# Performance work log

Hardware: AMD Instinct MI355X
Metric: run time of the kernel (lower is better)

Reference implementation:

```python
import jax, jax.numpy as jnp
import numpy as np

# dims: batch, time, in-feat, nodes, hidden, out-feat, filter taps, readout widths
BATCH, T, F, N, H, G = 8, 64, 8, 4096, 32, 32
K1, K2 = 3, 3
R1, R2 = 64, 8


def lsigf(h, S, x):
    """K-tap graph filter (LSIGF, E=1): h (Fout,K,Fin), S (N,N), x (B,Fin,N) -> (B,Fout,N)."""
    K = h.shape[1]
    xs = [x]
    for _ in range(K - 1):  # K is small and static
        xs.append(jnp.einsum('nm,bfm->bfn', S, xs[-1]))
    xk = jnp.stack(xs, axis=1)  # B,K,Fin,N
    return jnp.einsum('gkf,bkfn->bgn', h, xk)


def setup_inputs() -> dict:
    key = jax.random.key(0)
    ks = jax.random.split(key, 20)
    def p(k, shape, scale):
        return jax.random.normal(k, shape, dtype=jnp.float32) * scale
    x = jax.random.normal(ks[0], (BATCH, T, F, N), dtype=jnp.float32)
    z0 = jax.random.normal(ks[1], (BATCH, H, N), dtype=jnp.float32)  # random initial hidden state
    S = jax.random.normal(ks[2], (N, N), dtype=jnp.float32) / jnp.sqrt(jnp.float32(N))  # GSO, O(1) spectral norm
    sA = 1.0 / np.sqrt(K1 * F); sB = 1.0 / np.sqrt(K1 * H); sO = 1.0 / np.sqrt(K2 * H)
    return dict(
        x=x, z0=z0, S=S,
        # main hidden-state filters
        A=p(ks[3], (H, K1, F), sA), Bw=p(ks[4], (H, K1, H), sB), bz=p(ks[5], (H, 1), 0.1),
        # input (update) time-gate filters
        Ca=p(ks[6], (H, K1, F), sA), Cb=p(ks[7], (H, K1, H), sB), bc=p(ks[8], (H, 1), 0.1),
        # forget time-gate filters
        Da=p(ks[9], (H, K1, F), sA), Db=p(ks[10], (H, K1, H), sB), bd=p(ks[11], (H, 1), 0.1),
        # output graph filter
        Wout=p(ks[12], (G, K2, H), sO), bout=p(ks[13], (G, 1), 0.1),
        # local per-node readout MLP G -> R1 -> R2
        W1=p(ks[14], (R1, G), 1.0 / np.sqrt(G)), b1=p(ks[15], (R1,), 0.1),
        W2=p(ks[16], (R2, R1), 1.0 / np.sqrt(R1)), b2=p(ks[17], (R2,), 0.1),
    )


def reference(x, z0, S, A, Bw, bz, Ca, Cb, bc, Da, Db, bd, Wout, bout, W1, b1, W2, b2):
    Bsz = x.shape[0]
    xt_seq = jnp.moveaxis(x, 1, 0)  # T,B,F,N

    def step(z, xt):
        # scalar-per-(batch,time) gates: sigmoid of gate graph filters, pooled over nodes+features
        u = jax.nn.sigmoid(lsigf(Ca, S, xt) + lsigf(Cb, S, z) + bc).mean(axis=(1, 2))[:, None, None]
        f = jax.nn.sigmoid(lsigf(Da, S, xt) + lsigf(Db, S, z) + bd).mean(axis=(1, 2))[:, None, None]
        znew = jnp.tanh(u * lsigf(A, S, xt) + f * lsigf(Bw, S, z) + bz)
        return znew, znew

    _, zs = jax.lax.scan(step, z0, xt_seq)  # T,B,H,N
    z = jnp.moveaxis(zs, 0, 1).reshape(Bsz * T, H, N)
    yOut = jnp.tanh(lsigf(Wout, S, z) + bout).reshape(Bsz, T, G, N)  # nonlinearityOutput = tanh
    y = jnp.moveaxis(yOut, 2, 3)  # B,T,N,G  (local per-node readout)
    y = jax.nn.relu(y @ W1.T + b1) @ W2.T + b2  # B,T,N,R2
    return jnp.moveaxis(y, 3, 2)  # B,T,R2,N
```

## Files before the change

kernel.cpp:

```cpp
#include <hip/hip_runtime.h>
#include <hip/hip_bf16.h>
#include <cstdio>

typedef __attribute__((ext_vector_type(4))) float f32x4;
typedef __attribute__((ext_vector_type(8))) short bf16x8;

__device__ __forceinline__ short f2b(float f) {
  unsigned u = __builtin_bit_cast(unsigned, f);
  unsigned r = (u + 0x7FFFu + ((u >> 16) & 1u)) >> 16;
  return (short)r;
}
__device__ __forceinline__ float b2f(short s) {
  union { unsigned u; float f; } c;
  c.u = ((unsigned)(unsigned short)s) << 16;
  return c.f;
}
__device__ __forceinline__ float sigm(float x) { return 1.f / (1.f + __expf(-x)); }
__device__ __forceinline__ float tanh_f(float x) {
  float e = __expf(2.f * x);
  return 1.f - 2.f / (e + 1.f);
}

#define GLOAD16(gp, lp) \
  __builtin_amdgcn_global_load_lds((__attribute__((address_space(1))) const void*)(gp), \
                                   (__attribute__((address_space(3))) void*)(lp), 16, 0, 0)


__global__ void conv_k(const float* __restrict__ in, short* __restrict__ out, int n8) {
  int i = blockIdx.x * 256 + threadIdx.x;
  if (i >= n8) return;
  size_t base = (size_t)i * 8;
  f32x4 a = *(const f32x4*)(in + base), b = *(const f32x4*)(in + base + 4);
  bf16x8 v;
#pragma unroll
  for (int j = 0; j < 4; ++j) { v[j] = f2b(a[j]); v[4 + j] = f2b(b[j]); }
  *(bf16x8*)(out + base) = v;
}

__global__ void transpose_k(const float* __restrict__ in, short* __restrict__ out) {
  __shared__ float tile[32][33];
  int bx = blockIdx.x * 32, by = blockIdx.y * 32;
  int tx = threadIdx.x, ty = threadIdx.y;
  for (int i = ty; i < 32; i += 8)
    tile[i][tx] = in[(size_t)(by + i) * 4096 + bx + tx];
  __syncthreads();
  for (int i = ty; i < 32; i += 8)
    out[(size_t)(bx + i) * 4096 + by + tx] = f2b(tile[tx][i]);
}

template <int AF32>
__global__ __launch_bounds__(256) void gemm_big(const void* __restrict__ Av,
                                                const short* __restrict__ Bt,
                                                short* __restrict__ C,
                                                int K, int ldc) {
  __shared__ __align__(16) short Ab[2][128 * 64];
  __shared__ __align__(16) short Bb[2][128 * 64];
  const int tid = threadIdx.x, lane = tid & 63, w = tid >> 6;
  const int wm = w >> 1, wn = w & 1;
  const int r16 = lane & 15, g4 = lane >> 4;
  const size_t m0 = (size_t)blockIdx.y * 128, n0 = (size_t)blockIdx.x * 128;
  const int lrow8 = lane >> 3;
  const int lslot = (lane & 7) ^ lrow8;
  const int swz = r16 & 7;
  const int arow = tid >> 1, acol0 = (tid & 1) * 32, aslotb = (tid & 1) * 4;

  f32x4 acc[4][4];
#pragma unroll
  for (int mi = 0; mi < 4; ++mi)
#pragma unroll
    for (int ni = 0; ni < 4; ++ni) acc[mi][ni] = (f32x4)0.f;

  auto stageB = [&](int bs, int kt) {
#pragma unroll
    for (int i = 0; i < 4; ++i) {
      int chunk = w * 4 + i, row = chunk * 8 + lrow8;
      GLOAD16(&Bt[(size_t)(n0 + row) * K + kt + lslot * 8], &Bb[bs][chunk * 512]);
    }
  };
  auto stageA16 = [&](int bs, int kt) {
    const short* A = (const short*)Av;
#pragma unroll
    for (int i = 0; i < 4; ++i) {
      int chunk = w * 4 + i, row = chunk * 8 + lrow8;
      GLOAD16(&A[(size_t)(m0 + row) * K + kt + lslot * 8], &Ab[bs][chunk * 512]);
    }
  };
  auto writeA32 = [&](int bs, const f32x4* st) {
#pragma unroll
    for (int s = 0; s < 4; ++s) {
      bf16x8 v;
#pragma unroll
      for (int e = 0; e < 4; ++e) { v[e] = f2b(st[s * 2][e]); v[4 + e] = f2b(st[s * 2 + 1][e]); }
      int ps = (aslotb + s) ^ (arow & 7);
      *(bf16x8*)&Ab[bs][arow * 64 + ps * 8] = v;
    }
  };

  const float* A32 = (const float*)Av;
  if (AF32) {
    f32x4 st[8];
#pragma unroll
    for (int j = 0; j < 8; ++j)
      st[j] = *(const f32x4*)&A32[(m0 + arow) * (size_t)K + acol0 + j * 4];
    stageB(0, 0);
    writeA32(0, st);
  } else {
    stageA16(0, 0);
    stageB(0, 0);
  }
  __syncthreads();

  int cur = 0;
  for (int kt = 0; kt < K; kt += 64) {
    const bool nxt = (kt + 64 < K);
    f32x4 st[8];
    if (nxt) {
      if (AF32) {
#pragma unroll
        for (int j = 0; j < 8; ++j)
          st[j] = *(const f32x4*)&A32[(m0 + arow) * (size_t)K + kt + 64 + acol0 + j * 4];
      } else {
        stageA16(cur ^ 1, kt + 64);
      }
      stageB(cur ^ 1, kt + 64);
    }
#pragma unroll
    for (int ks = 0; ks < 2; ++ks) {
      const int so = ((ks * 4 + g4) ^ swz) * 8;
      bf16x8 af[4], bf[4];
#pragma unroll
      for (int i = 0; i < 4; ++i) {
        af[i] = *(const bf16x8*)&Ab[cur][(wm * 64 + i * 16 + r16) * 64 + so];
        bf[i] = *(const bf16x8*)&Bb[cur][(wn * 64 + i * 16 + r16) * 64 + so];
      }
#pragma unroll
      for (int mi = 0; mi < 4; ++mi)
#pragma unroll
        for (int ni = 0; ni < 4; ++ni)
          acc[mi][ni] = __builtin_amdgcn_mfma_f32_16x16x32_bf16(af[mi], bf[ni], acc[mi][ni], 0, 0, 0);
    }
    if (nxt && AF32) writeA32(cur ^ 1, st);
    __syncthreads();
    cur ^= 1;
  }
#pragma unroll
  for (int mi = 0; mi < 4; ++mi) {
#pragma unroll
    for (int ni = 0; ni < 4; ++ni) {
      size_t row0 = m0 + wm * 64 + mi * 16 + g4 * 4;
      size_t col  = n0 + wn * 64 + ni * 16 + r16;
#pragma unroll
      for (int r = 0; r < 4; ++r)
        C[(row0 + r) * (size_t)ldc + col] = f2b(acc[mi][ni][r]);
    }
  }
}

__global__ __launch_bounds__(512, 1) void step_fused(
    const short* __restrict__ zbuf, const short* __restrict__ Scat,
    const float* __restrict__ x, const short* __restrict__ xsh,
    const float* __restrict__ Ca, const float* __restrict__ Cb, const float* __restrict__ bc,
    const float* __restrict__ Da, const float* __restrict__ Db, const float* __restrict__ bd,
    const float* __restrict__ Af, const float* __restrict__ Bw,
    const float* __restrict__ Wout, const float* __restrict__ bout,
    const float* __restrict__ W1, const float* __restrict__ b1,
    const float* __restrict__ W2, const float* __restrict__ b2,
    float* __restrict__ zab, float* __restrict__ gacc,
    float* __restrict__ out, int t) {
  __shared__ __align__(16) char smem[118624];
  short* AbB = (short*)smem;
  short* BbB = (short*)(smem + 32768);
  short* Cs  = (short*)smem;
  short* zs  = (short*)(smem + 18432);
  float* Fu  = (float*)(smem + 49152);
  float* Fd  = (float*)(smem + 64512);
  float* Fb  = (float*)(smem + 79872);
  float* Fa  = (float*)(smem + 92160);
  float* Wc  = (float*)(smem + 95232);
  float* W1L = (float*)(smem + 107520);
  float* W2L = (float*)(smem + 115712);
  float* bcs   = (float*)(smem + 117760);
  float* bds   = (float*)(smem + 117888);
  float* boutL = (float*)(smem + 118144);
  float* b1L   = (float*)(smem + 118272);
  float* b2L   = (float*)(smem + 118528);
  float* red   = (float*)(smem + 118560);

  const int tid = threadIdx.x, lane = tid & 63, w = tid >> 6;
  const int wm = w >> 1, wn = w & 1;
  const int r16 = lane & 15, g4 = lane >> 4;
  const int lrow8 = lane >> 3;
  const int lslot = (lane & 7) ^ lrow8;
  const int swz = r16 & 7;
  const int mhalf = blockIdx.x >> 7, ntile = blockIdx.x & 127;
  const int m0 = mhalf << 7, n0 = ntile << 5;

  for (int i = tid; i < 3840; i += 512) {
    int j = i >> 5, h = i & 31; float fu, fd;
    if (j < 96) { int k = j >> 5, hh = j & 31;
      fu = Cb[(h * 3 + k) * 32 + hh]; fd = Db[(h * 3 + k) * 32 + hh]; }
    else { int jj = j - 96, k = jj >> 3, f = jj & 7;
      fu = Ca[(h * 3 + k) * 8 + f];  fd = Da[(h * 3 + k) * 8 + f]; }
    Fu[i] = fu; Fd[i] = fd;
  }
  for (int i = tid; i < 3072; i += 512) { int j = i >> 5, h = i & 31, k = j >> 5, hh = j & 31;
    Fb[i] = Bw[(h * 3 + k) * 32 + hh]; }
  for (int i = tid; i < 768;  i += 512) { int j = i >> 5, h = i & 31, k = j >> 3, f = j & 7;
    Fa[i] = Af[(h * 3 + k) * 8 + f]; }
  for (int i = tid; i < 3072; i += 512) { int j = i >> 5, g = i & 31, k = j >> 5, hh = j & 31;
    Wc[i] = Wout[(g * 3 + k) * 32 + hh]; }
  for (int i = tid; i < 2048; i += 512) { int r1 = i >> 5, g = i & 31; W1L[i] = W1[r1 * 32 + g]; }
  if (tid < 512) { int r1 = tid >> 3, r = tid & 7; W2L[tid] = W2[r * 64 + r1]; }
  if (tid < 32) { bcs[tid] = bc[tid]; bds[tid] = bd[tid]; boutL[tid] = bout[tid]; }
  if (tid < 64) b1L[tid] = b1[tid];
  if (tid < 8)  b2L[tid] = b2[tid];
  __syncthreads();

  const short* z = zbuf + (size_t)(t & 1) * 1048576;

  f32x4 acc[2][2];
  acc[0][0] = acc[0][1] = acc[1][0] = acc[1][1] = (f32x4)0.f;
  auto stage = [&](int bs, int kt) {
#pragma unroll
    for (int i = 0; i < 2; ++i) {
      int chunk = w * 2 + i, row = chunk * 8 + lrow8;
      GLOAD16(&z[(size_t)(m0 + row) * 4096 + kt + lslot * 8], &AbB[bs * 8192 + chunk * 512]);
    }
    { int row = w * 8 + lrow8;
      int grow = (row < 32) ? (n0 + row) : (4064 + n0 + row);
      GLOAD16(&Scat[(size_t)grow * 4096 + kt + lslot * 8], &BbB[bs * 4096 + w * 512]); }
  };
  stage(0, 0);
  __syncthreads();
  int cur = 0;
  for (int kt = 0; kt < 4096; kt += 64) {
    if (kt + 64 < 4096) stage(cur ^ 1, kt + 64);
#pragma unroll
    for (int ks = 0; ks < 2; ++ks) {
      const int so = ((ks * 4 + g4) ^ swz) * 8;
      bf16x8 af[2], bb[2];
#pragma unroll
      for (int i = 0; i < 2; ++i) {
        af[i] = *(const bf16x8*)&AbB[cur * 8192 + (wm * 32 + i * 16 + r16) * 64 + so];
        bb[i] = *(const bf16x8*)&BbB[cur * 4096 + (wn * 32 + i * 16 + r16) * 64 + so];
      }
#pragma unroll
      for (int mi = 0; mi < 2; ++mi)
#pragma unroll
        for (int ni = 0; ni < 2; ++ni)
          acc[mi][ni] = __builtin_amdgcn_mfma_f32_16x16x32_bf16(af[mi], bb[ni], acc[mi][ni], 0, 0, 0);
    }
    __syncthreads();
    cur ^= 1;
  }
#pragma unroll
  for (int mi = 0; mi < 2; ++mi)
#pragma unroll
    for (int ni = 0; ni < 2; ++ni) {
      int row0 = wm * 32 + mi * 16 + g4 * 4, col = wn * 32 + ni * 16 + r16;
#pragma unroll
      for (int rr = 0; rr < 4; ++rr)
        Cs[(row0 + rr) * 72 + col] = f2b(acc[mi][ni][rr]);
    }
  { int row = tid >> 2, c0 = (tid & 3) * 8;
    *(bf16x8*)&zs[row * 40 + c0] = *(const bf16x8*)&z[(size_t)(m0 + row) * 4096 + n0 + c0]; }
  __syncthreads();

  if (t >= 1 && tid < 128) {
    int b_loc = tid >> 5, nn = tid & 31;
    int b_glob = (mhalf << 2) + b_loc;
    f32x4 oa[8];
#pragma unroll
    for (int q = 0; q < 8; ++q) oa[q] = (f32x4)0.f;
    for (int j = 0; j < 96; ++j) {
      int k = j >> 5, hh = j & 31;
      float v = (k == 0) ? b2f(zs[(b_loc * 32 + hh) * 40 + nn])
                         : b2f(Cs[(b_loc * 32 + hh) * 72 + (k - 1) * 32 + nn]);
#pragma unroll
      for (int q = 0; q < 8; ++q) oa[q] += (*(const f32x4*)&Wc[j * 32 + q * 4]) * v;
    }
    f32x4 y[8];
#pragma unroll
    for (int q = 0; q < 8; ++q)
#pragma unroll
      for (int c = 0; c < 4; ++c) y[q][c] = tanh_f(oa[q][c] + boutL[q * 4 + c]);
    f32x4 o0 = { b2L[0], b2L[1], b2L[2], b2L[3] };
    f32x4 o1 = { b2L[4], b2L[5], b2L[6], b2L[7] };
    for (int r1 = 0; r1 < 64; ++r1) {
      f32x4 p = y[0] * (*(const f32x4*)&W1L[r1 * 32]);
#pragma unroll
      for (int q = 1; q < 8; ++q) p += y[q] * (*(const f32x4*)&W1L[r1 * 32 + q * 4]);
      float hv = b1L[r1] + p[0] + p[1] + p[2] + p[3];
      hv = fmaxf(hv, 0.f);
      o0 += (*(const f32x4*)&W2L[r1 * 8]) * hv;
      o1 += (*(const f32x4*)&W2L[r1 * 8 + 4]) * hv;
    }
    size_t obase = ((size_t)(b_glob * 64 + (t - 1)) * 8) * 4096 + n0 + nn;
#pragma unroll
    for (int rr = 0; rr < 4; ++rr) {
      out[obase + (size_t)rr * 4096]       = o0[rr];
      out[obase + (size_t)(4 + rr) * 4096] = o1[rr];
    }
  }

  if (t < 64) {
    int nn = tid & 31; int q = tid >> 5; int b_loc = q >> 2; int h0 = (q & 3) * 8;
    int b_glob = (mhalf << 2) + b_loc;
    int n = n0 + nn;
    f32x4 zaA = (f32x4)0.f, zaB = (f32x4)0.f, zbA = (f32x4)0.f, zbB = (f32x4)0.f;
    f32x4 guA = *(const f32x4*)&bcs[h0], guB = *(const f32x4*)&bcs[h0 + 4];
    f32x4 gdA = *(const f32x4*)&bds[h0], gdB = *(const f32x4*)&bds[h0 + 4];
    for (int j = 0; j < 96; ++j) {
      int k = j >> 5, hh = j & 31;
      float v = (k == 0) ? b2f(zs[(b_loc * 32 + hh) * 40 + nn])
                         : b2f(Cs[(b_loc * 32 + hh) * 72 + (k - 1) * 32 + nn]);
      guA += (*(const f32x4*)&Fu[j * 32 + h0]) * v;  guB += (*(const f32x4*)&Fu[j * 32 + h0 + 4]) * v;
      gdA += (*(const f32x4*)&Fd[j * 32 + h0]) * v;  gdB += (*(const f32x4*)&Fd[j * 32 + h0 + 4]) * v;
      zbA += (*(const f32x4*)&Fb[j * 32 + h0]) * v;  zbB += (*(const f32x4*)&Fb[j * 32 + h0 + 4]) * v;
    }
    size_t xr = ((size_t)b_glob * 64 + t) * 8;
    for (int j = 0; j < 24; ++j) {
      int k = j >> 3, f = j & 7;
      float v = (k == 0) ? x[(xr + f) * 4096 + n]
                         : b2f(xsh[(xr + f) * 8192 + (size_t)(k - 1) * 4096 + n]);
      guA += (*(const f32x4*)&Fu[(96 + j) * 32 + h0]) * v;  guB += (*(const f32x4*)&Fu[(96 + j) * 32 + h0 + 4]) * v;
      gdA += (*(const f32x4*)&Fd[(96 + j) * 32 + h0]) * v;  gdB += (*(const f32x4*)&Fd[(96 + j) * 32 + h0 + 4]) * v;
      zaA += (*(const f32x4*)&Fa[j * 32 + h0]) * v;         zaB += (*(const f32x4*)&Fa[j * 32 + h0 + 4]) * v;
    }
    float su = 0.f, sd = 0.f;
    size_t zr = (size_t)(b_glob * 32 + h0) * 4096 + n;
#pragma unroll
    for (int i = 0; i < 4; ++i) {
      su += sigm(guA[i]) + sigm(guB[i]);
      sd += sigm(gdA[i]) + sigm(gdB[i]);
      zab[zr + (size_t)i * 4096]                 = zaA[i];
      zab[zr + (size_t)(4 + i) * 4096]           = zaB[i];
      zab[1048576 + zr + (size_t)i * 4096]       = zbA[i];
      zab[1048576 + zr + (size_t)(4 + i) * 4096] = zbB[i];
    }
#pragma unroll
    for (int off = 32; off; off >>= 1) { su += __shfl_down(su, off); sd += __shfl_down(sd, off); }
    if (lane == 0) { red[w * 2] = su; red[w * 2 + 1] = sd; }
    __syncthreads();
    if (tid < 4) {
      int par = t & 1, bg = (mhalf << 2) + tid;
      atomicAdd(&gacc[par * 16 + bg],     red[4 * tid] + red[4 * tid + 2]);
      atomicAdd(&gacc[par * 16 + 8 + bg], red[4 * tid + 1] + red[4 * tid + 3]);
    }
  }
}

__global__ __launch_bounds__(256) void update_kernel(
    const float* __restrict__ zab, float* __restrict__ gacc,
    const float* __restrict__ bz, short* __restrict__ zout, int t) {
  const int par = t & 1;
  if (blockIdx.x == 0 && threadIdx.x < 16) gacc[(par ^ 1) * 16 + threadIdx.x] = 0.f;
  size_t idx = (size_t)blockIdx.x * 256 + threadIdx.x;
  size_t base = idx * 8;
  int row = (int)(base >> 12);
  int b = row >> 5, h = row & 31;
  float u  = gacc[par * 16 + b]     * (1.f / 131072.f);
  float fg = gacc[par * 16 + 8 + b] * (1.f / 131072.f);
  float bzv = bz[h];
  f32x4 za0 = *(const f32x4*)(zab + base),           za1 = *(const f32x4*)(zab + base + 4);
  f32x4 zb0 = *(const f32x4*)(zab + 1048576 + base), zb1 = *(const f32x4*)(zab + 1048576 + base + 4);
  bf16x8 ov;
#pragma unroll
  for (int i = 0; i < 4; ++i) {
    ov[i]     = f2b(tanh_f(u * za0[i] + fg * zb0[i] + bzv));
    ov[4 + i] = f2b(tanh_f(u * za1[i] + fg * zb1[i] + bzv));
  }
  *(bf16x8*)(zout + base) = ov;
}

extern "C" void kernel_launch(void* const* d_in, const int* in_sizes, int n_in,
                              void* d_out, int out_size, void* d_ws, size_t ws_size,
                              hipStream_t stream) {
  const float* x    = (const float*)d_in[0];
  const float* z0   = (const float*)d_in[1];
  const float* S    = (const float*)d_in[2];
  const float* Af   = (const float*)d_in[3];
  const float* Bw   = (const float*)d_in[4];
  const float* bz   = (const float*)d_in[5];
  const float* Ca   = (const float*)d_in[6];
  const float* Cb   = (const float*)d_in[7];
  const float* bc   = (const float*)d_in[8];
  const float* Da   = (const float*)d_in[9];
  const float* Db   = (const float*)d_in[10];
  const float* bd   = (const float*)d_in[11];
  const float* Wout = (const float*)d_in[12];
  const float* bo   = (const float*)d_in[13];
  const float* W1   = (const float*)d_in[14];
  const float* b1   = (const float*)d_in[15];
  const float* W2   = (const float*)d_in[16];
  const float* b2   = (const float*)d_in[17];
  float* out = (float*)d_out;

  char* w = (char*)d_ws;
  short* Scat = (short*)w; w += (size_t)8192 * 4096 * 2;
  short* xsh  = (short*)w; w += (size_t)4096 * 8192 * 2;
  short* zbuf = (short*)w; w += (size_t)2 * 1048576 * 2;
  float* zab  = (float*)w; w += (size_t)2 * 1048576 * 4;
  float* gacc = (float*)w; w += 256;
  size_t need = (size_t)(w - (char*)d_ws);
  if (ws_size < need) {
    fprintf(stderr, "kernel_launch: WS TOO SMALL need=%zu have=%zu -- NOT LAUNCHING\n",
            need, ws_size);
    return;
  }

  short* STt = xsh;

  conv_k<<<512, 256, 0, stream>>>(z0, zbuf, 131072);
  conv_k<<<8192, 256, 0, stream>>>(S, Scat, 2097152);
  transpose_k<<<dim3(128, 128), dim3(32, 8), 0, stream>>>(S, STt);
  gemm_big<0><<<dim3(32, 32), 256, 0, stream>>>(Scat, STt, Scat + (size_t)4096 * 4096, 4096, 4096);
  gemm_big<1><<<dim3(64, 32), 256, 0, stream>>>(x, Scat, xsh, 4096, 8192);
  hipMemsetAsync(gacc, 0, 256, stream);

  for (int t = 0; t <= 64; ++t) {
    short* znxt = zbuf + (size_t)((t + 1) & 1) * 1048576;
    step_fused<<<256, 512, 0, stream>>>(zbuf, Scat, x, xsh,
                                        Ca, Cb, bc, Da, Db, bd, Af, Bw,
                                        Wout, bo, W1, b1, W2, b2,
                                        zab, gacc, out, t);
    if (t < 64)
      update_kernel<<<512, 256, 0, stream>>>(zab, gacc, bz, znxt, t);
  }
}
```

Before: 6.905 ms.

## Triple-buffer step kernel GEMM loads and simplify precompute GEMM staging

```diff
diff --git a/kernel.cpp b/kernel.cpp
--- a/kernel.cpp
+++ b/kernel.cpp
@@ -49,20 +49,17 @@
 }
 
 template <int AF32>
-__global__ __launch_bounds__(256) void gemm_big(const void* __restrict__ Av,
+__global__ __launch_bounds__(256) void gemm_pre(const void* __restrict__ Av,
                                                 const short* __restrict__ Bt,
                                                 short* __restrict__ C,
                                                 int K, int ldc) {
-  __shared__ __align__(16) short Ab[2][128 * 64];
-  __shared__ __align__(16) short Bb[2][128 * 64];
-  const int tid = threadIdx.x, lane = tid & 63, w = tid >> 6;
-  const int wm = w >> 1, wn = w & 1;
+  __shared__ __align__(16) short As[128][72];
+  __shared__ __align__(16) short Bs[128][72];
+  const int tid = threadIdx.x;
+  const int lane = tid & 63, wave = tid >> 6;
+  const int wm = wave >> 1, wn = wave & 1;
+  const size_t m0 = (size_t)blockIdx.y * 128, n0 = (size_t)blockIdx.x * 128;
   const int r16 = lane & 15, g4 = lane >> 4;
-  const size_t m0 = (size_t)blockIdx.y * 128, n0 = (size_t)blockIdx.x * 128;
-  const int lrow8 = lane >> 3;
-  const int lslot = (lane & 7) ^ lrow8;
-  const int swz = r16 & 7;
-  const int arow = tid >> 1, acol0 = (tid & 1) * 32, aslotb = (tid & 1) * 4;
 
   f32x4 acc[4][4];
 #pragma unroll
@@ -70,78 +67,42 @@
 #pragma unroll
     for (int ni = 0; ni < 4; ++ni) acc[mi][ni] = (f32x4)0.f;
 
-  auto stageB = [&](int bs, int kt) {
-#pragma unroll
-    for (int i = 0; i < 4; ++i) {
-      int chunk = w * 4 + i, row = chunk * 8 + lrow8;
-      GLOAD16(&Bt[(size_t)(n0 + row) * K + kt + lslot * 8], &Bb[bs][chunk * 512]);
-    }
-  };
-  auto stageA16 = [&](int bs, int kt) {
-    const short* A = (const short*)Av;
-#pragma unroll
-    for (int i = 0; i < 4; ++i) {
-      int chunk = w * 4 + i, row = chunk * 8 + lrow8;
-      GLOAD16(&A[(size_t)(m0 + row) * K + kt + lslot * 8], &Ab[bs][chunk * 512]);
-    }
-  };
-  auto writeA32 = [&](int bs, const f32x4* st) {
-#pragma unroll
-    for (int s = 0; s < 4; ++s) {
-      bf16x8 v;
-#pragma unroll
-      for (int e = 0; e < 4; ++e) { v[e] = f2b(st[s * 2][e]); v[4 + e] = f2b(st[s * 2 + 1][e]); }
-      int ps = (aslotb + s) ^ (arow & 7);
-      *(bf16x8*)&Ab[bs][arow * 64 + ps * 8] = v;
-    }
-  };
-
-  const float* A32 = (const float*)Av;
-  if (AF32) {
-    f32x4 st[8];
-#pragma unroll
-    for (int j = 0; j < 8; ++j)
-      st[j] = *(const f32x4*)&A32[(m0 + arow) * (size_t)K + acol0 + j * 4];
-    stageB(0, 0);
-    writeA32(0, st);
-  } else {
-    stageA16(0, 0);
-    stageB(0, 0);
-  }
-  __syncthreads();
-
-  int cur = 0;
   for (int kt = 0; kt < K; kt += 64) {
-    const bool nxt = (kt + 64 < K);
-    f32x4 st[8];
-    if (nxt) {
+#pragma unroll
+    for (int r = 0; r < 4; ++r) {
+      int idx = r * 256 + tid;
+      int row = idx >> 3;
+      int kin = (idx & 7) * 8;
       if (AF32) {
-#pragma unroll
-        for (int j = 0; j < 8; ++j)
-          st[j] = *(const f32x4*)&A32[(m0 + arow) * (size_t)K + kt + 64 + acol0 + j * 4];
+        const float* A = (const float*)Av;
+        const float* p = &A[(m0 + row) * (size_t)K + kt + kin];
+        f32x4 a = *(const f32x4*)p, b = *(const f32x4*)(p + 4);
+        bf16x8 v;
+#pragma unroll
+        for (int j = 0; j < 4; ++j) { v[j] = f2b(a[j]); v[4 + j] = f2b(b[j]); }
+        *(bf16x8*)&As[row][kin] = v;
       } else {
-        stageA16(cur ^ 1, kt + 64);
+        const short* A = (const short*)Av;
+        *(bf16x8*)&As[row][kin] = *(const bf16x8*)&A[(m0 + row) * (size_t)K + kt + kin];
       }
-      stageB(cur ^ 1, kt + 64);
-    }
+      *(bf16x8*)&Bs[row][kin] = *(const bf16x8*)&Bt[(n0 + row) * (size_t)K + kt + kin];
+    }
+    __syncthreads();
 #pragma unroll
     for (int ks = 0; ks < 2; ++ks) {
-      const int so = ((ks * 4 + g4) ^ swz) * 8;
-      bf16x8 af[4], bf[4];
+      bf16x8 af[4], bfr[4];
 #pragma unroll
       for (int i = 0; i < 4; ++i) {
-        af[i] = *(const bf16x8*)&Ab[cur][(wm * 64 + i * 16 + r16) * 64 + so];
-        bf[i] = *(const bf16x8*)&Bb[cur][(wn * 64 + i * 16 + r16) * 64 + so];
+        af[i]  = *(const bf16x8*)&As[wm * 64 + i * 16 + r16][ks * 32 + g4 * 8];
+        bfr[i] = *(const bf16x8*)&Bs[wn * 64 + i * 16 + r16][ks * 32 + g4 * 8];
       }
 #pragma unroll
       for (int mi = 0; mi < 4; ++mi)
 #pragma unroll
         for (int ni = 0; ni < 4; ++ni)
-          acc[mi][ni] = __builtin_amdgcn_mfma_f32_16x16x32_bf16(af[mi], bf[ni], acc[mi][ni], 0, 0, 0);
-    }
-    if (nxt && AF32) writeA32(cur ^ 1, st);
+          acc[mi][ni] = __builtin_amdgcn_mfma_f32_16x16x32_bf16(af[mi], bfr[ni], acc[mi][ni], 0, 0, 0);
+    }
     __syncthreads();
-    cur ^= 1;
   }
 #pragma unroll
   for (int mi = 0; mi < 4; ++mi) {
@@ -167,24 +128,24 @@
     const float* __restrict__ W2, const float* __restrict__ b2,
     float* __restrict__ zab, float* __restrict__ gacc,
     float* __restrict__ out, int t) {
-  __shared__ __align__(16) char smem[118624];
+  __shared__ __align__(16) char smem[143072];
   short* AbB = (short*)smem;
-  short* BbB = (short*)(smem + 32768);
+  short* BbB = (short*)(smem + 49152);
   short* Cs  = (short*)smem;
   short* zs  = (short*)(smem + 18432);
-  float* Fu  = (float*)(smem + 49152);
-  float* Fd  = (float*)(smem + 64512);
-  float* Fb  = (float*)(smem + 79872);
-  float* Fa  = (float*)(smem + 92160);
-  float* Wc  = (float*)(smem + 95232);
-  float* W1L = (float*)(smem + 107520);
-  float* W2L = (float*)(smem + 115712);
-  float* bcs   = (float*)(smem + 117760);
-  float* bds   = (float*)(smem + 117888);
-  float* boutL = (float*)(smem + 118144);
-  float* b1L   = (float*)(smem + 118272);
-  float* b2L   = (float*)(smem + 118528);
-  float* red   = (float*)(smem + 118560);
+  float* Fu  = (float*)(smem + 73728);
+  float* Fd  = (float*)(smem + 89088);
+  float* Fb  = (float*)(smem + 104448);
+  float* Fa  = (float*)(smem + 116736);
+  float* Wc  = (float*)(smem + 119808);
+  float* W1L = (float*)(smem + 132096);
+  float* W2L = (float*)(smem + 140288);
+  float* bcs   = (float*)(smem + 142336);
+  float* bds   = (float*)(smem + 142464);
+  float* boutL = (float*)(smem + 142592);
+  float* b1L   = (float*)(smem + 142720);
+  float* b2L   = (float*)(smem + 142976);
+  float* red   = (float*)(smem + 143008);
 
   const int tid = threadIdx.x, lane = tid & 63, w = tid >> 6;
   const int wm = w >> 1, wn = w & 1;
@@ -231,18 +192,22 @@
       GLOAD16(&Scat[(size_t)grow * 4096 + kt + lslot * 8], &BbB[bs * 4096 + w * 512]); }
   };
   stage(0, 0);
-  __syncthreads();
-  int cur = 0;
-  for (int kt = 0; kt < 4096; kt += 64) {
-    if (kt + 64 < 4096) stage(cur ^ 1, kt + 64);
+  stage(1, 64);
+  for (int i = 0; i < 64; ++i) {
+    if (i < 63) { asm volatile("s_waitcnt vmcnt(3)" ::: "memory"); }
+    else        { asm volatile("s_waitcnt vmcnt(0)" ::: "memory"); }
+    __builtin_amdgcn_s_barrier();
+    __builtin_amdgcn_sched_barrier(0);
+    if (i + 2 < 64) stage((i + 2) % 3, (i + 2) * 64);
+    const int cur = i % 3;
 #pragma unroll
     for (int ks = 0; ks < 2; ++ks) {
       const int so = ((ks * 4 + g4) ^ swz) * 8;
       bf16x8 af[2], bb[2];
 #pragma unroll
-      for (int i = 0; i < 2; ++i) {
-        af[i] = *(const bf16x8*)&AbB[cur * 8192 + (wm * 32 + i * 16 + r16) * 64 + so];
-        bb[i] = *(const bf16x8*)&BbB[cur * 4096 + (wn * 32 + i * 16 + r16) * 64 + so];
+      for (int ii = 0; ii < 2; ++ii) {
+        af[ii] = *(const bf16x8*)&AbB[cur * 8192 + (wm * 32 + ii * 16 + r16) * 64 + so];
+        bb[ii] = *(const bf16x8*)&BbB[cur * 4096 + (wn * 32 + ii * 16 + r16) * 64 + so];
       }
 #pragma unroll
       for (int mi = 0; mi < 2; ++mi)
@@ -250,9 +215,9 @@
         for (int ni = 0; ni < 2; ++ni)
           acc[mi][ni] = __builtin_amdgcn_mfma_f32_16x16x32_bf16(af[mi], bb[ni], acc[mi][ni], 0, 0, 0);
     }
-    __syncthreads();
-    cur ^= 1;
-  }
+  }
+  __syncthreads();
+
 #pragma unroll
   for (int mi = 0; mi < 2; ++mi)
 #pragma unroll
@@ -414,8 +379,8 @@
   conv_k<<<512, 256, 0, stream>>>(z0, zbuf, 131072);
   conv_k<<<8192, 256, 0, stream>>>(S, Scat, 2097152);
   transpose_k<<<dim3(128, 128), dim3(32, 8), 0, stream>>>(S, STt);
-  gemm_big<0><<<dim3(32, 32), 256, 0, stream>>>(Scat, STt, Scat + (size_t)4096 * 4096, 4096, 4096);
-  gemm_big<1><<<dim3(64, 32), 256, 0, stream>>>(x, Scat, xsh, 4096, 8192);
+  gemm_pre<0><<<dim3(32, 32), 256, 0, stream>>>(Scat, STt, Scat + (size_t)4096 * 4096, 4096, 4096);
+  gemm_pre<1><<<dim3(64, 32), 256, 0, stream>>>(x, Scat, xsh, 4096, 8192);
   hipMemsetAsync(gacc, 0, 256, stream);
 
   for (int t = 0; t <= 64; ++t) {
```

Result: faster. 6.178 ms, median of 2 (-10.5%).
